# Kernel optimization log

Measured on AMD Instinct MI355X. Metric: run time of the kernel, lower is better.

## Reference

```python
import jax, jax.numpy as jnp
import numpy as np

B, S, D, H = 2, 2048, 1024, 16
DK = D // H
SCALE = DK ** 0.5


def setup_inputs() -> dict:
    key = jax.random.key(0)
    ks = jax.random.split(key, 5)
    std = 1.0 / np.sqrt(D)
    return {
        "x": jax.random.normal(ks[0], (B, S, D), dtype=jnp.float32),
        "Wq": jax.random.normal(ks[1], (D, D), dtype=jnp.float32) * std,
        "Wk": jax.random.normal(ks[2], (D, D), dtype=jnp.float32) * std,
        "Wv": jax.random.normal(ks[3], (D, D), dtype=jnp.float32) * std,
        "Wo": jax.random.normal(ks[4], (D, D), dtype=jnp.float32) * std,
    }


def _split_heads(t):
    # [B, S, D] -> [B, H, S, DK]
    b, s, d = t.shape
    return t.reshape(b, s, H, DK).transpose(0, 2, 1, 3)


def reference(x, Wq, Wk, Wv, Wo):
    b, s, d = x.shape
    q = _split_heads(x @ Wq)
    k = _split_heads(x @ Wk)
    v = _split_heads(x @ Wv)
    # scores: [B, H, S, S]
    score = jnp.einsum("bhqd,bhkd->bhqk", q, k)
    causal = jnp.tril(jnp.ones((s, s), dtype=bool))[None, None]
    score = jnp.where(causal, score, -jnp.inf)
    attn = jax.nn.softmax(score / SCALE, axis=-1)
    out = jnp.einsum("bhqk,bhkd->bhqd", attn, v)
    out = out.transpose(0, 2, 1, 3).reshape(b, s, d)
    return out @ Wo
```

## Files before the change

### kernel.cpp

```cpp
#include <hip/hip_runtime.h>
#include <hip/hip_bf16.h>

typedef __bf16 bf16;
typedef __bf16 bf16x4 __attribute__((ext_vector_type(4)));
typedef __bf16 bf16x8 __attribute__((ext_vector_type(8)));
typedef float f32x4 __attribute__((ext_vector_type(4)));

#define MFMA16(a, b, c) __builtin_amdgcn_mfma_f32_16x16x32_bf16((a), (b), (c), 0, 0, 0)

__device__ __forceinline__ void async16(const void* g, void* l) {
  typedef const unsigned int __attribute__((address_space(1))) * GP;
  typedef unsigned int __attribute__((address_space(3))) * LP;
  __builtin_amdgcn_global_load_lds((GP)g, (LP)l, 16, 0, 0);
}

__global__ __launch_bounds__(256) void prep(
    const float* __restrict__ w0, const float* __restrict__ w1,
    const float* __restrict__ w2, const float* __restrict__ w3,
    const float* __restrict__ x, bf16* __restrict__ wtOut,
    bf16* __restrict__ xOut) {
  const int t = threadIdx.x;
  if (blockIdx.z == 4) {
    size_t base = ((size_t)(blockIdx.y * 16 + blockIdx.x)) * 16384;
#pragma unroll
    for (int p = 0; p < 16; ++p) {
      size_t i = base + (size_t)(p * 256 + t) * 4;
      f32x4 v = *(const f32x4*)&x[i];
      bf16 o[4];
#pragma unroll
      for (int j = 0; j < 4; ++j) o[j] = (bf16)v[j];
      *(ulong1*)&xOut[i] = *(ulong1*)o;
    }
    return;
  }
  __shared__ __align__(16) float tile[64][68];
  const float* src = (blockIdx.z == 0) ? w0 : (blockIdx.z == 1) ? w1
                   : (blockIdx.z == 2) ? w2 : w3;
  bf16* dst = wtOut + (size_t)blockIdx.z * (1024u * 1024u);
  const int bx = blockIdx.x, by = blockIdx.y;
#pragma unroll
  for (int p = 0; p < 4; ++p) {
    int idx = t + p * 256;
    int r = idx >> 4, c4 = idx & 15;
    *(f32x4*)&tile[r][c4 * 4] =
        *(const f32x4*)&src[(size_t)(by * 64 + r) * 1024 + bx * 64 + c4 * 4];
  }
  __syncthreads();
#pragma unroll
  for (int p = 0; p < 2; ++p) {
    int idx = t + p * 256;
    int rn = idx >> 3, c8 = idx & 7;
    bf16x8 v;
#pragma unroll
    for (int i = 0; i < 8; ++i) v[i] = (bf16)tile[c8 * 8 + i][rn];
    *(bf16x8*)&dst[(size_t)(bx * 64 + rn) * 1024 + by * 64 + c8 * 8] = v;
  }
}

template <typename OutT, int NI>
__global__ __launch_bounds__(256, 4) void gemm_bt(
    const bf16* __restrict__ A, const bf16* __restrict__ Bt,
    OutT* __restrict__ C, int btStrideZ, int cStrideZ, float scaleZ0,
    bf16* __restrict__ vtOut) {
  constexpr int XT = 1024 / (NI * 32);
  const int bid = blockIdx.x;
  const int rr = bid & 7, tt = bid >> 3;
  const int xb = tt % XT, yb = (tt / XT) * 8 + rr;
  const int zi = blockIdx.y;

  const int tid = threadIdx.x;
  const int wave = tid >> 6, lane = tid & 63;
  const int quad = lane >> 4, l16 = lane & 15;
  const int wm = wave >> 1, wn = wave & 1;
  const int m0 = yb * 128, n0 = xb * (NI * 32);
  const bf16* Bz = Bt + (size_t)zi * (size_t)btStrideZ;
  OutT* Cz = C + (size_t)zi * (size_t)cStrideZ;
  const float sc = (zi == 0) ? scaleZ0 : 1.0f;

  __shared__ __align__(16) bf16 lsA[2][128 * 32];
  __shared__ __align__(16) bf16 lsB[2][NI * 32 * 32];

  const int lrow = lane >> 2;
  const int cgX = (lane & 3) ^ ((lrow >> 1) & 3);
  const int fR = (l16 >> 1) & 3;

  f32x4 acc[4][NI];
#pragma unroll
  for (int i = 0; i < 4; ++i)
#pragma unroll
    for (int j = 0; j < NI; ++j) acc[i][j] = (f32x4){0.f, 0.f, 0.f, 0.f};

#pragma unroll
  for (int c = 0; c < 2; ++c) {
    int chunk = wave * 2 + c;
    int row = chunk * 16 + lrow;
    async16(&A[(size_t)(m0 + row) * 1024 + cgX * 8], &lsA[0][chunk * 512]);
  }
#pragma unroll
  for (int c = 0; c < NI / 2; ++c) {
    int chunk = wave * (NI / 2) + c;
    int row = chunk * 16 + lrow;
    async16(&Bz[(size_t)(n0 + row) * 1024 + cgX * 8], &lsB[0][chunk * 512]);
  }
  __syncthreads();

  for (int it = 0; it < 32; ++it) {
    const int cur = it & 1;
    if (it < 31) {
      int k0n = (it + 1) * 32;
#pragma unroll
      for (int c = 0; c < 2; ++c) {
        int chunk = wave * 2 + c;
        int row = chunk * 16 + lrow;
        async16(&A[(size_t)(m0 + row) * 1024 + k0n + cgX * 8],
                &lsA[cur ^ 1][chunk * 512]);
      }
#pragma unroll
      for (int c = 0; c < NI / 2; ++c) {
        int chunk = wave * (NI / 2) + c;
        int row = chunk * 16 + lrow;
        async16(&Bz[(size_t)(n0 + row) * 1024 + k0n + cgX * 8],
                &lsB[cur ^ 1][chunk * 512]);
      }
    }

    bf16x8 af[4], bfr[NI];
#pragma unroll
    for (int i = 0; i < 4; ++i) {
      int ra = wm * 64 + i * 16 + l16;
      af[i] = *(const bf16x8*)&lsA[cur][ra * 32 + ((quad ^ fR) * 8)];
    }
#pragma unroll
    for (int ni = 0; ni < NI; ++ni) {
      int rb = wn * (NI * 16) + ni * 16 + l16;
      bfr[ni] = *(const bf16x8*)&lsB[cur][rb * 32 + ((quad ^ fR) * 8)];
    }
#pragma unroll
    for (int mi = 0; mi < 4; ++mi)
#pragma unroll
      for (int ni = 0; ni < NI; ++ni)
        acc[mi][ni] = MFMA16(af[mi], bfr[ni], acc[mi][ni]);

    __syncthreads();
  }

  if (zi == 2 && vtOut != nullptr) {
#pragma unroll
    for (int mi = 0; mi < 4; ++mi)
#pragma unroll
      for (int ni = 0; ni < NI; ++ni) {
        int col = n0 + wn * (NI * 16) + ni * 16 + l16;
        int hd = col >> 6, d = col & 63;
        int row = m0 + wm * 64 + mi * 16 + quad * 4;
        int b = row >> 11, s = row & 2047;
        int s32 = s & 31;
        int sp = (s & ~31) + ((s32 & 12) << 1) + ((s32 >> 4) << 2);
        bf16 o[4];
#pragma unroll
        for (int r = 0; r < 4; ++r) o[r] = (bf16)acc[mi][ni][r];
        *(ulong1*)&vtOut[((size_t)(b * 16 + hd) * 64 + d) * 2048 + sp] =
            *(ulong1*)o;
      }
  } else {
#pragma unroll
    for (int mi = 0; mi < 4; ++mi)
#pragma unroll
      for (int ni = 0; ni < NI; ++ni) {
        int col = n0 + wn * (NI * 16) + ni * 16 + l16;
#pragma unroll
        for (int r = 0; r < 4; ++r) {
          int row = m0 + wm * 64 + mi * 16 + quad * 4 + r;
          Cz[(size_t)row * 1024 + col] = (OutT)(acc[mi][ni][r] * sc);
        }
      }
  }
}

__global__ __launch_bounds__(256, 3) void attn_fwd(
    const bf16* __restrict__ Q, const bf16* __restrict__ K,
    const bf16* __restrict__ Vt, bf16* __restrict__ O) {
  const int bid = blockIdx.x;
  const int xcd = bid & 7;
  const int i = bid >> 3;
  const int g4 = i & 3;
  const int j = i >> 2;
  const int qt = (j < 8) ? j : (23 - j);
  const int bh = xcd * 4 + g4;
  const int h = bh & 15, b = bh >> 4;
  const int tid = threadIdx.x;
  const int wave = tid >> 6, lane = tid & 63;
  const int quad = lane >> 4, l16 = lane & 15;

  __shared__ __align__(16) bf16 SMEM[24576];
  bf16* Qs = &SMEM[16384];

  const size_t base = ((size_t)b * 2048) * 1024 + (size_t)h * 64;
  const bf16* Qb = Q + base;
  const bf16* Kb = K + base;
  const bf16* Vtb = Vt + ((size_t)(b * 16 + h)) * 64 * 2048;
  bf16* Ob = O + base;

  const int lrow = lane >> 3;
  const int cgX = (lane & 7) ^ lrow;

#pragma unroll
  for (int c = 0; c < 4; ++c) {
    int chunk = wave * 4 + c;
    int row = chunk * 8 + lrow;
    async16(&Qb[(size_t)(qt * 128 + row) * 1024 + cgX * 8], &Qs[chunk * 512]);
  }
#pragma unroll
  for (int c = 0; c < 2; ++c) {
    int chunk = wave * 2 + c;
    int row = chunk * 8 + lrow;
    async16(&Kb[(size_t)row * 1024 + cgX * 8], &SMEM[chunk * 512]);
    async16(&Vtb[(size_t)row * 2048 + cgX * 8], &SMEM[4096 + chunk * 512]);
  }
  __syncthreads();

  bf16x8 aq[2][2];
#pragma unroll
  for (int g = 0; g < 2; ++g)
#pragma unroll
    for (int ks = 0; ks < 2; ++ks) {
      int row = wave * 32 + g * 16 + l16;
      aq[g][ks] =
          *(const bf16x8*)&Qs[row * 64 + (((ks * 4 + quad) ^ (l16 & 7)) * 8)];
    }

  const float NEG_INF = -__builtin_inff();
  f32x4 lsv[2];
  f32x4 Oacc[2][4];
#pragma unroll
  for (int g = 0; g < 2; ++g) {
    lsv[g] = (f32x4){0.f, 0.f, 0.f, 0.f};
#pragma unroll
    for (int nt = 0; nt < 4; ++nt) Oacc[g][nt] = (f32x4){0.f, 0.f, 0.f, 0.f};
  }

  const int ktmax = 2 * qt + 1;
  const int ktd = 2 * qt + (wave >> 1);

  for (int kt = 0; kt <= ktmax; ++kt) {
    const int cur = kt & 1;
    if (kt < ktmax) {
      const int ns = (cur ^ 1) * 8192;
#pragma unroll
      for (int c = 0; c < 2; ++c) {
        int chunk = wave * 2 + c;
        int row = chunk * 8 + lrow;
        async16(&Kb[(size_t)((kt + 1) * 64 + row) * 1024 + cgX * 8],
                &SMEM[ns + chunk * 512]);
        async16(&Vtb[(size_t)row * 2048 + (kt + 1) * 64 + cgX * 8],
                &SMEM[ns + 4096 + chunk * 512]);
      }
    }

    const int ko = cur * 8192;
    const int vo = ko + 4096;

    if (kt <= ktd) {
      const int cb = (kt - 2 * qt) * 64;
      const bool diag = (kt == ktd);
#pragma unroll
      for (int a = 0; a < 2; ++a) {
        f32x4 s[2][2];
#pragma unroll
        for (int t = 0; t < 2; ++t) {
          const int nt = 2 * a + t;
          const int row = nt * 16 + l16;
          bf16x8 bk0 =
              *(const bf16x8*)&SMEM[ko + row * 64 + ((quad ^ (l16 & 7)) * 8)];
          bf16x8 bk1 = *(const bf16x8*)&SMEM[ko + row * 64 +
                                             (((4 + quad) ^ (l16 & 7)) * 8)];
          __builtin_amdgcn_s_setprio(1);
#pragma unroll
          for (int g = 0; g < 2; ++g) {
            f32x4 sv = (f32x4){0.f, 0.f, 0.f, 0.f};
            sv = MFMA16(bk0, aq[g][0], sv);
            sv = MFMA16(bk1, aq[g][1], sv);
            s[g][t] = sv;
          }
          __builtin_amdgcn_s_setprio(0);
        }

        if (diag) {
#pragma unroll
          for (int g = 0; g < 2; ++g) {
            const int q_rel = wave * 32 + g * 16 + l16;
#pragma unroll
            for (int t = 0; t < 2; ++t) {
              const int kb = cb + (2 * a + t) * 16 + quad * 4;
#pragma unroll
              for (int r = 0; r < 4; ++r)
                if (kb + r > q_rel) s[g][t][r] = NEG_INF;
            }
          }
        }

        bf16x8 apf[2];
#pragma unroll
        for (int g = 0; g < 2; ++g) {
#pragma unroll
          for (int t = 0; t < 2; ++t) {
#pragma unroll
            for (int r = 0; r < 4; ++r)
              s[g][t][r] = __builtin_amdgcn_exp2f(s[g][t][r]);
            lsv[g] += s[g][t];
          }
          bf16x4 c0 = __builtin_convertvector(s[g][0], bf16x4);
          bf16x4 c1 = __builtin_convertvector(s[g][1], bf16x4);
#pragma unroll
          for (int i2 = 0; i2 < 4; ++i2) {
            apf[g][i2] = c0[i2];
            apf[g][4 + i2] = c1[i2];
          }
        }

#pragma unroll
        for (int nt = 0; nt < 4; ++nt) {
          const int R = nt * 16 + l16;
          bf16x8 bvf = *(const bf16x8*)&SMEM[vo + R * 64 +
                                             (((a * 4 + quad) ^ (l16 & 7)) *
                                              8)];
          __builtin_amdgcn_s_setprio(1);
#pragma unroll
          for (int g = 0; g < 2; ++g)
            Oacc[g][nt] = MFMA16(apf[g], bvf, Oacc[g][nt]);
          __builtin_amdgcn_s_setprio(0);
        }
      }
    }

    __syncthreads();
  }

  float ls[2];
#pragma unroll
  for (int g = 0; g < 2; ++g) {
    float a_ = lsv[g][0] + lsv[g][1] + lsv[g][2] + lsv[g][3];
    a_ += __shfl_xor(a_, 16, 64);
    a_ += __shfl_xor(a_, 32, 64);
    ls[g] = a_;
  }
  float rl[2][4];
#pragma unroll
  for (int g = 0; g < 2; ++g)
#pragma unroll
    for (int r = 0; r < 4; ++r)
      rl[g][r] = 1.f / __shfl(ls[g], quad * 4 + r, 64);
#pragma unroll
  for (int g = 0; g < 2; ++g)
#pragma unroll
    for (int nt = 0; nt < 4; ++nt)
#pragma unroll
      for (int r = 0; r < 4; ++r) {
        int row = qt * 128 + wave * 32 + g * 16 + quad * 4 + r;
        Ob[(size_t)row * 1024 + nt * 16 + l16] =
            (bf16)(Oacc[g][nt][r] * rl[g][r]);
      }
}

extern "C" void kernel_launch(void* const* d_in, const int* in_sizes, int n_in,
                              void* d_out, int out_size, void* d_ws,
                              size_t ws_size, hipStream_t stream) {
  (void)in_sizes; (void)n_in; (void)out_size; (void)ws_size;
  const float* x  = (const float*)d_in[0];
  const float* Wq = (const float*)d_in[1];
  const float* Wk = (const float*)d_in[2];
  const float* Wv = (const float*)d_in[3];
  const float* Wo = (const float*)d_in[4];
  float* out = (float*)d_out;

  bf16* ws = (bf16*)d_ws;
  const size_t WELEM = 1024u * 1024u;
  const size_t TELEM = 4096u * 1024u;
  bf16* wt  = ws;
  bf16* xbf = ws + 4 * WELEM;
  bf16* q   = xbf + TELEM;
  bf16* k   = q + TELEM;
  bf16* vt  = k + TELEM;
  bf16* ao  = vt + TELEM;

  const float QSCALE = 0.125f * 1.44269504088896340736f;

  prep<<<dim3(16, 16, 5), 256, 0, stream>>>(Wq, Wk, Wv, Wo, x, wt, xbf);
  gemm_bt<bf16, 4><<<dim3(256, 3), 256, 0, stream>>>(
      xbf, wt, q, (int)WELEM, (int)TELEM, QSCALE, vt);
  attn_fwd<<<dim3(512), 256, 0, stream>>>(q, k, vt, ao);
  gemm_bt<float, 2><<<dim3(512, 1), 256, 0, stream>>>(
      ao, wt + 3 * WELEM, out, 0, 0, 1.0f, nullptr);
}
```

Before: 167.3 us.

## Split attention into 64-row query tiles with intra-block key-split reduction

Attention blocks now cover 64 query rows instead of 128. The four waves split as two query halves times two key halves of each 64-key tile, and the key-half partial outputs and row sums are combined through shared memory at the end. This doubles the grid to 1024 blocks, reorders query tiles for causal load balance, shrinks shared memory and raises the occupancy hint to 4. The aim is better CU occupancy and load balance under the causal mask, at the cost of re-streaming K/V for each smaller query tile plus an extra reduction step.

```diff
diff --git a/kernel.cpp b/kernel.cpp
--- a/kernel.cpp
+++ b/kernel.cpp
@@ -176,7 +176,7 @@
   }
 }
 
-__global__ __launch_bounds__(256, 3) void attn_fwd(
+__global__ __launch_bounds__(256, 4) void attn_fwd(
     const bf16* __restrict__ Q, const bf16* __restrict__ K,
     const bf16* __restrict__ Vt, bf16* __restrict__ O) {
   const int bid = blockIdx.x;
@@ -184,14 +184,17 @@
   const int i = bid >> 3;
   const int g4 = i & 3;
   const int j = i >> 2;
-  const int qt = (j < 8) ? j : (23 - j);
+  const int a = j & 7, bq = j >> 3;
+  const int qt = (bq < 2) ? (31 - 2 * a - bq) : (2 * a + (bq & 1));
   const int bh = xcd * 4 + g4;
   const int h = bh & 15, b = bh >> 4;
   const int tid = threadIdx.x;
   const int wave = tid >> 6, lane = tid & 63;
   const int quad = lane >> 4, l16 = lane & 15;
-
-  __shared__ __align__(16) bf16 SMEM[24576];
+  const int qh = wave >> 1;
+  const int kh = wave & 1;
+
+  __shared__ __align__(16) bf16 SMEM[20480];
   bf16* Qs = &SMEM[16384];
 
   const size_t base = ((size_t)b * 2048) * 1024 + (size_t)h * 64;
@@ -204,15 +207,10 @@
   const int cgX = (lane & 7) ^ lrow;
 
 #pragma unroll
-  for (int c = 0; c < 4; ++c) {
-    int chunk = wave * 4 + c;
-    int row = chunk * 8 + lrow;
-    async16(&Qb[(size_t)(qt * 128 + row) * 1024 + cgX * 8], &Qs[chunk * 512]);
-  }
-#pragma unroll
   for (int c = 0; c < 2; ++c) {
     int chunk = wave * 2 + c;
     int row = chunk * 8 + lrow;
+    async16(&Qb[(size_t)(qt * 64 + row) * 1024 + cgX * 8], &Qs[chunk * 512]);
     async16(&Kb[(size_t)row * 1024 + cgX * 8], &SMEM[chunk * 512]);
     async16(&Vtb[(size_t)row * 2048 + cgX * 8], &SMEM[4096 + chunk * 512]);
   }
@@ -223,7 +221,7 @@
   for (int g = 0; g < 2; ++g)
 #pragma unroll
     for (int ks = 0; ks < 2; ++ks) {
-      int row = wave * 32 + g * 16 + l16;
+      int row = qh * 32 + g * 16 + l16;
       aq[g][ks] =
           *(const bf16x8*)&Qs[row * 64 + (((ks * 4 + quad) ^ (l16 & 7)) * 8)];
     }
@@ -238,12 +236,9 @@
     for (int nt = 0; nt < 4; ++nt) Oacc[g][nt] = (f32x4){0.f, 0.f, 0.f, 0.f};
   }
 
-  const int ktmax = 2 * qt + 1;
-  const int ktd = 2 * qt + (wave >> 1);
-
-  for (int kt = 0; kt <= ktmax; ++kt) {
+  for (int kt = 0; kt <= qt; ++kt) {
     const int cur = kt & 1;
-    if (kt < ktmax) {
+    if (kt < qt) {
       const int ns = (cur ^ 1) * 8192;
 #pragma unroll
       for (int c = 0; c < 2; ++c) {
@@ -258,107 +253,123 @@
 
     const int ko = cur * 8192;
     const int vo = ko + 4096;
-
-    if (kt <= ktd) {
-      const int cb = (kt - 2 * qt) * 64;
-      const bool diag = (kt == ktd);
-#pragma unroll
-      for (int a = 0; a < 2; ++a) {
-        f32x4 s[2][2];
+    const bool diag = (kt == qt);
+
+    if (!(diag && kh == 1 && qh == 0)) {
+      f32x4 s[2][2];
+#pragma unroll
+      for (int t = 0; t < 2; ++t) {
+        const int row = kh * 32 + t * 16 + l16;
+        bf16x8 bk0 =
+            *(const bf16x8*)&SMEM[ko + row * 64 + ((quad ^ (l16 & 7)) * 8)];
+        bf16x8 bk1 = *(const bf16x8*)&SMEM[ko + row * 64 +
+                                           (((4 + quad) ^ (l16 & 7)) * 8)];
+        __builtin_amdgcn_s_setprio(1);
+#pragma unroll
+        for (int g = 0; g < 2; ++g) {
+          f32x4 sv = (f32x4){0.f, 0.f, 0.f, 0.f};
+          sv = MFMA16(bk0, aq[g][0], sv);
+          sv = MFMA16(bk1, aq[g][1], sv);
+          s[g][t] = sv;
+        }
+        __builtin_amdgcn_s_setprio(0);
+      }
+
+      if (diag) {
+#pragma unroll
+        for (int g = 0; g < 2; ++g) {
+          const int q_rel = qh * 32 + g * 16 + l16;
+#pragma unroll
+          for (int t = 0; t < 2; ++t) {
+            const int kb = kh * 32 + t * 16 + quad * 4;
+#pragma unroll
+            for (int r = 0; r < 4; ++r)
+              if (kb + r > q_rel) s[g][t][r] = NEG_INF;
+          }
+        }
+      }
+
+      bf16x8 apf[2];
+#pragma unroll
+      for (int g = 0; g < 2; ++g) {
 #pragma unroll
         for (int t = 0; t < 2; ++t) {
-          const int nt = 2 * a + t;
-          const int row = nt * 16 + l16;
-          bf16x8 bk0 =
-              *(const bf16x8*)&SMEM[ko + row * 64 + ((quad ^ (l16 & 7)) * 8)];
-          bf16x8 bk1 = *(const bf16x8*)&SMEM[ko + row * 64 +
-                                             (((4 + quad) ^ (l16 & 7)) * 8)];
-          __builtin_amdgcn_s_setprio(1);
-#pragma unroll
-          for (int g = 0; g < 2; ++g) {
-            f32x4 sv = (f32x4){0.f, 0.f, 0.f, 0.f};
-            sv = MFMA16(bk0, aq[g][0], sv);
-            sv = MFMA16(bk1, aq[g][1], sv);
-            s[g][t] = sv;
-          }
-          __builtin_amdgcn_s_setprio(0);
-        }
-
-        if (diag) {
-#pragma unroll
-          for (int g = 0; g < 2; ++g) {
-            const int q_rel = wave * 32 + g * 16 + l16;
-#pragma unroll
-            for (int t = 0; t < 2; ++t) {
-              const int kb = cb + (2 * a + t) * 16 + quad * 4;
-#pragma unroll
-              for (int r = 0; r < 4; ++r)
-                if (kb + r > q_rel) s[g][t][r] = NEG_INF;
-            }
-          }
-        }
-
-        bf16x8 apf[2];
-#pragma unroll
-        for (int g = 0; g < 2; ++g) {
-#pragma unroll
-          for (int t = 0; t < 2; ++t) {
-#pragma unroll
-            for (int r = 0; r < 4; ++r)
-              s[g][t][r] = __builtin_amdgcn_exp2f(s[g][t][r]);
-            lsv[g] += s[g][t];
-          }
-          bf16x4 c0 = __builtin_convertvector(s[g][0], bf16x4);
-          bf16x4 c1 = __builtin_convertvector(s[g][1], bf16x4);
-#pragma unroll
-          for (int i2 = 0; i2 < 4; ++i2) {
-            apf[g][i2] = c0[i2];
-            apf[g][4 + i2] = c1[i2];
-          }
-        }
-
-#pragma unroll
-        for (int nt = 0; nt < 4; ++nt) {
-          const int R = nt * 16 + l16;
-          bf16x8 bvf = *(const bf16x8*)&SMEM[vo + R * 64 +
-                                             (((a * 4 + quad) ^ (l16 & 7)) *
-                                              8)];
-          __builtin_amdgcn_s_setprio(1);
-#pragma unroll
-          for (int g = 0; g < 2; ++g)
-            Oacc[g][nt] = MFMA16(apf[g], bvf, Oacc[g][nt]);
-          __builtin_amdgcn_s_setprio(0);
-        }
+#pragma unroll
+          for (int r = 0; r < 4; ++r)
+            s[g][t][r] = __builtin_amdgcn_exp2f(s[g][t][r]);
+          lsv[g] += s[g][t];
+        }
+        bf16x4 c0 = __builtin_convertvector(s[g][0], bf16x4);
+        bf16x4 c1 = __builtin_convertvector(s[g][1], bf16x4);
+#pragma unroll
+        for (int i2 = 0; i2 < 4; ++i2) {
+          apf[g][i2] = c0[i2];
+          apf[g][4 + i2] = c1[i2];
+        }
+      }
+
+#pragma unroll
+      for (int nt = 0; nt < 4; ++nt) {
+        const int R = nt * 16 + l16;
+        bf16x8 bvf = *(const bf16x8*)&SMEM[vo + R * 64 +
+                                           (((kh * 4 + quad) ^ (l16 & 7)) *
+                                            8)];
+        __builtin_amdgcn_s_setprio(1);
+#pragma unroll
+        for (int g = 0; g < 2; ++g)
+          Oacc[g][nt] = MFMA16(apf[g], bvf, Oacc[g][nt]);
+        __builtin_amdgcn_s_setprio(0);
       }
     }
 
     __syncthreads();
   }
 
-  float ls[2];
-#pragma unroll
-  for (int g = 0; g < 2; ++g) {
-    float a_ = lsv[g][0] + lsv[g][1] + lsv[g][2] + lsv[g][3];
-    a_ += __shfl_xor(a_, 16, 64);
-    a_ += __shfl_xor(a_, 32, 64);
-    ls[g] = a_;
-  }
-  float rl[2][4];
-#pragma unroll
-  for (int g = 0; g < 2; ++g)
-#pragma unroll
-    for (int r = 0; r < 4; ++r)
-      rl[g][r] = 1.f / __shfl(ls[g], quad * 4 + r, 64);
-#pragma unroll
-  for (int g = 0; g < 2; ++g)
-#pragma unroll
-    for (int nt = 0; nt < 4; ++nt)
-#pragma unroll
-      for (int r = 0; r < 4; ++r) {
-        int row = qt * 128 + wave * 32 + g * 16 + quad * 4 + r;
-        Ob[(size_t)row * 1024 + nt * 16 + l16] =
-            (bf16)(Oacc[g][nt][r] * rl[g][r]);
-      }
+  float* F = (float*)SMEM;
+  const int qoff = qh * 2560;
+  if (kh == 1) {
+#pragma unroll
+    for (int g = 0; g < 2; ++g) {
+#pragma unroll
+      for (int nt = 0; nt < 4; ++nt)
+        *(f32x4*)&F[qoff + (g * 4 + nt) * 256 + lane * 4] = Oacc[g][nt];
+      *(f32x4*)&F[qoff + 2048 + g * 256 + lane * 4] = lsv[g];
+    }
+  }
+  __syncthreads();
+  if (kh == 0) {
+#pragma unroll
+    for (int g = 0; g < 2; ++g) {
+#pragma unroll
+      for (int nt = 0; nt < 4; ++nt)
+        Oacc[g][nt] += *(const f32x4*)&F[qoff + (g * 4 + nt) * 256 + lane * 4];
+      lsv[g] += *(const f32x4*)&F[qoff + 2048 + g * 256 + lane * 4];
+    }
+    float ls[2];
+#pragma unroll
+    for (int g = 0; g < 2; ++g) {
+      float a_ = lsv[g][0] + lsv[g][1] + lsv[g][2] + lsv[g][3];
+      a_ += __shfl_xor(a_, 16, 64);
+      a_ += __shfl_xor(a_, 32, 64);
+      ls[g] = a_;
+    }
+    float rl[2][4];
+#pragma unroll
+    for (int g = 0; g < 2; ++g)
+#pragma unroll
+      for (int r = 0; r < 4; ++r)
+        rl[g][r] = 1.f / __shfl(ls[g], quad * 4 + r, 64);
+#pragma unroll
+    for (int g = 0; g < 2; ++g)
+#pragma unroll
+      for (int nt = 0; nt < 4; ++nt)
+#pragma unroll
+        for (int r = 0; r < 4; ++r) {
+          int row = qt * 64 + qh * 32 + g * 16 + quad * 4 + r;
+          Ob[(size_t)row * 1024 + nt * 16 + l16] =
+              (bf16)(Oacc[g][nt][r] * rl[g][r]);
+        }
+  }
 }
 
 extern "C" void kernel_launch(void* const* d_in, const int* in_sizes, int n_in,
@@ -387,7 +398,7 @@
   prep<<<dim3(16, 16, 5), 256, 0, stream>>>(Wq, Wk, Wv, Wo, x, wt, xbf);
   gemm_bt<bf16, 4><<<dim3(256, 3), 256, 0, stream>>>(
       xbf, wt, q, (int)WELEM, (int)TELEM, QSCALE, vt);
-  attn_fwd<<<dim3(512), 256, 0, stream>>>(q, k, vt, ao);
+  attn_fwd<<<dim3(1024), 256, 0, stream>>>(q, k, vt, ao);
   gemm_bt<float, 2><<<dim3(512, 1), 256, 0, stream>>>(
       ao, wt + 3 * WELEM, out, 0, 0, 1.0f, nullptr);
 }
```

Result: faster. 160.0 us, median of 3 (-4.3%).
